# Kernel tuning notes

Hardware: AMD Instinct MI355X
Metric: run time of the kernel (lower is better)

Reference implementation:

```python
import jax, jax.numpy as jnp
import numpy as np

D_MODEL = 768
N_HEADS = 12
HEAD_DIM = D_MODEL // N_HEADS
FFN_DIM = 3072
MAX_WAVELENGTH = 10000.0
ROPE_PERCENT = 0.5
NORM_EPS = 1e-5


def setup_inputs() -> dict:
    key = jax.random.key(0)
    ks = jax.random.split(key, 12)
    B, C, S = 2, 16, 128
    init = lambda k, shape: (jax.random.normal(k, shape, dtype=jnp.float32) * 0.02)
    return {
        "hidden_state": jax.random.normal(ks[0], (B, C, S, D_MODEL), dtype=jnp.float32),
        "wq": init(ks[1], (D_MODEL, D_MODEL)), "bq": jnp.zeros((D_MODEL,), jnp.float32),
        "wk": init(ks[2], (D_MODEL, D_MODEL)), "bk": jnp.zeros((D_MODEL,), jnp.float32),
        "wv": init(ks[3], (D_MODEL, D_MODEL)), "bv": jnp.zeros((D_MODEL,), jnp.float32),
        "wo": init(ks[4], (D_MODEL, D_MODEL)), "bo": jnp.zeros((D_MODEL,), jnp.float32),
        "attn_biases": init(ks[5], (N_HEADS, 2)),
        "ln1_g": jnp.ones((D_MODEL,), jnp.float32), "ln1_b": jnp.zeros((D_MODEL,), jnp.float32),
        "ln3_g": jnp.ones((D_MODEL,), jnp.float32), "ln3_b": jnp.zeros((D_MODEL,), jnp.float32),
        "w1": init(ks[6], (D_MODEL, FFN_DIM)), "b1": jnp.zeros((FFN_DIM,), jnp.float32),
        "w2": init(ks[7], (FFN_DIM, D_MODEL)), "b2": jnp.zeros((D_MODEL,), jnp.float32),
    }


def _layernorm(x, g, b):
    mu = jnp.mean(x, axis=-1, keepdims=True)
    var = jnp.mean(jnp.square(x - mu), axis=-1, keepdims=True)
    return (x - mu) * jax.lax.rsqrt(var + NORM_EPS) * g + b


def _apply_p_rope(x, positions):
    # x: [B, H, T, head_dim]; p-RoPE: only rope_percent of frequency bands rotate.
    half = HEAD_DIM // 2
    rope_angles = int(ROPE_PERCENT * HEAD_DIM) // 2  # 16
    fraction = 2.0 * jnp.arange(rope_angles, dtype=jnp.float32) / HEAD_DIM
    timescale = jnp.concatenate([
        MAX_WAVELENGTH ** fraction,
        jnp.full((half - rope_angles,), jnp.inf, dtype=jnp.float32),
    ])  # [half]
    angles = positions[:, None].astype(jnp.float32) / timescale[None, :]  # [T, half]
    sin = jnp.sin(angles)[None, None]  # [1,1,T,half]
    cos = jnp.cos(angles)[None, None]
    x1, x2 = jnp.split(x, 2, axis=-1)
    return jnp.concatenate([x1 * cos - x2 * sin, x2 * cos + x1 * sin], axis=-1)


def _forward(hidden_state, wq, bq, wk, bk, wv, bv, wo, bo, attn_biases,
             ln1_g, ln1_b, ln3_g, ln3_b, w1, b1, w2, b2):
    B, C, S, D = hidden_state.shape
    T = C * S
    flat = hidden_state.reshape(B, T, D)

    # --- attention sublayer (pre-norm) ---
    ni = _layernorm(flat, ln1_g, ln1_b)
    scaling = HEAD_DIM ** -0.5
    q = (ni @ wq + bq) * scaling
    k = ni @ wk + bk
    v = ni @ wv + bv
    to_heads = lambda t: t.reshape(B, T, N_HEADS, HEAD_DIM).transpose(0, 2, 1, 3)
    q, k, v = to_heads(q), to_heads(k), to_heads(v)  # [B,H,T,hd]

    positions = jnp.arange(T)
    k = _apply_p_rope(k, positions)
    q = _apply_p_rope(q, positions)

    scores = jnp.einsum("bhtd,bhsd->bhts", q, k)  # [B,H,T,T]
    variate_ids = positions // S
    same = (variate_ids[:, None] == variate_ids[None, :]).astype(scores.dtype)  # [T,T]
    variate_bias = (same[None, :, :] * attn_biases[:, 0][:, None, None]
                    + (1.0 - same[None, :, :]) * attn_biases[:, 1][:, None, None])  # [H,T,T]
    scores = scores + variate_bias[None]
    probs = jax.nn.softmax(scores, axis=-1)
    attn = jnp.einsum("bhts,bhsd->bhtd", probs, v)
    attn = attn.transpose(0, 2, 1, 3).reshape(B, T, D)
    attn = attn @ wo + bo

    flat = flat + attn  # residual (pre-norm -> no post-norm here)

    # --- feed-forward sublayer (pre-norm) ---
    ff_in = _layernorm(flat, ln3_g, ln3_b)
    ff = jax.nn.gelu(ff_in @ w1 + b1, approximate=False) @ w2 + b2
    flat = flat + ff

    return flat.reshape(B, C, S, D)


def reference(hidden_state, wq, bq, wk, bk, wv, bv, wo, bo, attn_biases,
              ln1_g, ln1_b, ln3_g, ln3_b, w1, b1, w2, b2):
    return _forward(hidden_state, wq, bq, wk, bk, wv, bv, wo, bo, attn_biases,
                    ln1_g, ln1_b, ln3_g, ln3_b, w1, b1, w2, b2)
```

## Files before the change

kernel.cpp:

```cpp
#include <hip/hip_runtime.h>
#include <cmath>


typedef __bf16 bf16_t;
typedef bf16_t bf16x8 __attribute__((ext_vector_type(8)));
typedef float floatx4 __attribute__((ext_vector_type(4)));

#define MFMA(a, b, c) __builtin_amdgcn_mfma_f32_16x16x32_bf16((a), (b), (c), 0, 0, 0)
#define LOG2E 1.44269504088896340736f

__device__ __forceinline__ bf16_t f2bf(float f) { return (bf16_t)f; }

__device__ __forceinline__ void g2l16(const void* g, void* l) {
  __builtin_amdgcn_global_load_lds(
      (const __attribute__((address_space(1))) unsigned int*)g,
      (__attribute__((address_space(3))) unsigned int*)l, 16, 0, 0);
}

__device__ __forceinline__ void lds_fence() {
  asm volatile("s_waitcnt lgkmcnt(0)" ::: "memory");
}

struct PrepP {
  const float *wq, *wk, *wv, *wo, *w1, *w2;
  bf16_t *wqkvT, *woT, *w1T, *w2T;
  const float *hs, *g1, *be1;
  bf16_t* ni;
};

__global__ __launch_bounds__(256) void k_prep(PrepP p) {
  __shared__ float shm[32 * 33];
  const int bid = blockIdx.x;
  if (bid < 6912) {
    const float* in;
    bf16_t* out;
    int R, C, tx, ty;
    if (bid < 2304) {
      int m = bid / 576, lo = bid % 576;
      in = (m == 0) ? p.wq : (m == 1) ? p.wk : (m == 2) ? p.wv : p.wo;
      out = (m < 3) ? p.wqkvT + (size_t)m * 768 * 768 : p.woT;
      R = 768; C = 768; tx = lo % 24; ty = lo / 24;
    } else if (bid < 4608) {
      int lo = bid - 2304;
      in = p.w1; out = p.w1T; R = 768; C = 3072; tx = lo % 96; ty = lo / 96;
    } else {
      int lo = bid - 4608;
      in = p.w2; out = p.w2T; R = 3072; C = 768; tx = lo % 24; ty = lo / 24;
    }
    const int c0 = tx * 32, r0 = ty * 32;
    const int lx = threadIdx.x & 31, ly = threadIdx.x >> 5;
#pragma unroll
    for (int p4 = 0; p4 < 4; p4++) {
      int r = ly + p4 * 8;
      shm[r * 33 + lx] = in[(size_t)(r0 + r) * C + c0 + lx];
    }
    __syncthreads();
#pragma unroll
    for (int p4 = 0; p4 < 4; p4++) {
      int r = ly + p4 * 8;
      out[(size_t)(c0 + r) * R + r0 + lx] = f2bf(shm[lx * 33 + r]);
    }
  } else {
    const int row = bid - 6912;
    const float* xr = p.hs + (size_t)row * 768;
    const int t = threadIdx.x;
    float v0 = xr[t], v1 = xr[t + 256], v2 = xr[t + 512];
    float s = v0 + v1 + v2;
    float s2 = v0 * v0 + v1 * v1 + v2 * v2;
#pragma unroll
    for (int off = 32; off; off >>= 1) {
      s += __shfl_xor(s, off);
      s2 += __shfl_xor(s2, off);
    }
    const int w = t >> 6;
    if ((t & 63) == 0) { shm[w] = s; shm[4 + w] = s2; }
    __syncthreads();
    s = shm[0] + shm[1] + shm[2] + shm[3];
    s2 = shm[4] + shm[5] + shm[6] + shm[7];
    const float mu = s * (1.0f / 768.0f);
    const float var = s2 * (1.0f / 768.0f) - mu * mu;
    const float rstd = rsqrtf(var + 1e-5f);
    bf16_t* orow = p.ni + (size_t)row * 768;
    orow[t]       = f2bf((v0 - mu) * rstd * p.g1[t]       + p.be1[t]);
    orow[t + 256] = f2bf((v1 - mu) * rstd * p.g1[t + 256] + p.be1[t + 256]);
    orow[t + 512] = f2bf((v2 - mu) * rstd * p.g1[t + 512] + p.be1[t + 512]);
  }
}

__global__ __launch_bounds__(256) void k_layernorm(
    const float* __restrict__ x, const float* __restrict__ g,
    const float* __restrict__ b, bf16_t* __restrict__ out) {
  const int row = blockIdx.x;
  const float* xr = x + (size_t)row * 768;
  const int t = threadIdx.x;
  float v0 = xr[t], v1 = xr[t + 256], v2 = xr[t + 512];
  float s = v0 + v1 + v2;
  float s2 = v0 * v0 + v1 * v1 + v2 * v2;
#pragma unroll
  for (int off = 32; off; off >>= 1) {
    s += __shfl_xor(s, off);
    s2 += __shfl_xor(s2, off);
  }
  __shared__ float ra[4], rb[4];
  const int w = t >> 6;
  if ((t & 63) == 0) { ra[w] = s; rb[w] = s2; }
  __syncthreads();
  s = ra[0] + ra[1] + ra[2] + ra[3];
  s2 = rb[0] + rb[1] + rb[2] + rb[3];
  const float mu = s * (1.0f / 768.0f);
  const float var = s2 * (1.0f / 768.0f) - mu * mu;
  const float rstd = rsqrtf(var + 1e-5f);
  bf16_t* orow = out + (size_t)row * 768;
  orow[t]       = f2bf((v0 - mu) * rstd * g[t]       + b[t]);
  orow[t + 256] = f2bf((v1 - mu) * rstd * g[t + 256] + b[t + 256]);
  orow[t + 512] = f2bf((v2 - mu) * rstd * g[t + 512] + b[t + 512]);
}

struct GemmP {
  const bf16_t* A;
  const bf16_t* Bt;
  int M, N, K, mode;
  const float* bias0;
  const float* bias1;
  const float* bias2;
  float* outF;
  bf16_t* outB0;
  bf16_t* outB1;
  bf16_t* outB2;
};

__global__ __launch_bounds__(256, 2) void k_gemm(GemmP p) {
  __shared__ bf16_t lds[32768];
  const int tid = threadIdx.x;
  const int lane = tid & 63, wave = tid >> 6;
  const int quad = lane >> 4, l15 = lane & 15;
  const int wm = (wave >> 1) * 64, wn = (wave & 1) * 64;
  const int m0 = blockIdx.y * 128, n0 = blockIdx.x * 128;

  const char* gA[4];
  const char* gB[4];
#pragma unroll
  for (int pp = 0; pp < 4; pp++) {
    int slot = wave * 256 + pp * 64 + lane;
    int r = slot >> 3;
    int c8 = ((slot & 7) ^ (r & 7)) << 3;
    gA[pp] = (const char*)(p.A + (size_t)(m0 + r) * p.K + c8);
    gB[pp] = (const char*)(p.Bt + (size_t)(n0 + r) * p.K + c8);
  }

  int offA[4], offB[4];
#pragma unroll
  for (int i = 0; i < 4; i++) {
    int ra = wm + i * 16 + l15;
    offA[i] = ra * 64 + ((quad * 8) ^ ((ra & 7) << 3));
    int rb = wn + i * 16 + l15;
    offB[i] = rb * 64 + ((quad * 8) ^ ((rb & 7) << 3));
  }

  const floatx4 z4 = {0.f, 0.f, 0.f, 0.f};
  floatx4 acc[4][4];
#pragma unroll
  for (int i = 0; i < 4; i++)
#pragma unroll
    for (int j = 0; j < 4; j++) acc[i][j] = z4;

  const int KT = p.K >> 6;
  {
    bf16_t* A0 = lds + wave * 2048;
    bf16_t* B0 = lds + 16384 + wave * 2048;
#pragma unroll
    for (int pp = 0; pp < 4; pp++) {
      g2l16(gA[pp], A0 + pp * 512);
      g2l16(gB[pp], B0 + pp * 512);
    }
  }
  __syncthreads();

  for (int kt = 0; kt < KT; kt++) {
    const int cur = kt & 1;
    if (kt + 1 < KT) {
      const size_t kb = (size_t)(kt + 1) * 128;
      bf16_t* A1 = lds + (cur ^ 1) * 8192 + wave * 2048;
      bf16_t* B1 = lds + 16384 + (cur ^ 1) * 8192 + wave * 2048;
#pragma unroll
      for (int pp = 0; pp < 4; pp++) {
        g2l16(gA[pp] + kb, A1 + pp * 512);
        g2l16(gB[pp] + kb, B1 + pp * 512);
      }
    }
    const bf16_t* A0 = lds + cur * 8192;
    const bf16_t* B0 = lds + 16384 + cur * 8192;
#pragma unroll
    for (int ks = 0; ks < 2; ks++) {
      bf16x8 af[4], bfr[4];
#pragma unroll
      for (int i = 0; i < 4; i++) {
        af[i] = *(const bf16x8*)(A0 + (offA[i] ^ (ks * 32)));
        bfr[i] = *(const bf16x8*)(B0 + (offB[i] ^ (ks * 32)));
      }
#pragma unroll
      for (int i = 0; i < 4; i++)
#pragma unroll
        for (int j = 0; j < 4; j++) acc[i][j] = MFMA(af[i], bfr[j], acc[i][j]);
    }
    __syncthreads();
  }

  char* scr = (char*)lds + wave * 16384;

  if (p.mode == 0) {
    const int gnw = n0 + wn;
    const int region = gnw / 768;
    const int rem = gnw - region * 768;
    const int h = rem >> 6;
    const int b = (m0 + wm) >> 11;
    const int t0 = (m0 + wm) & 2047;
    const float* bias = (region == 0) ? p.bias0 : (region == 1 ? p.bias1 : p.bias2);
    float bb[4];
#pragma unroll
    for (int j = 0; j < 4; j++) bb[j] = bias[h * 64 + j * 16 + l15];
    bf16_t* sb = (bf16_t*)scr;
    if (region < 2) {
      const float scale = (region == 0) ? 0.125f * LOG2E : 1.0f;
      const float inv_ts = exp2f(-(float)l15 * (13.287712379549449f / 32.0f));
#pragma unroll
      for (int i = 0; i < 4; i++) {
#pragma unroll
        for (int reg = 0; reg < 4; reg++) {
          int tl = i * 16 + quad * 4 + reg;
          float sn, cs;
          __sincosf((float)(t0 + tl) * inv_ts, &sn, &cs);
          float v0 = (acc[i][0][reg] + bb[0]) * scale;
          float v1 = (acc[i][1][reg] + bb[1]) * scale;
          float v2 = (acc[i][2][reg] + bb[2]) * scale;
          float v3 = (acc[i][3][reg] + bb[3]) * scale;
          sb[tl * 72 + l15]      = f2bf(v0 * cs - v2 * sn);
          sb[tl * 72 + 16 + l15] = f2bf(v1);
          sb[tl * 72 + 32 + l15] = f2bf(v2 * cs + v0 * sn);
          sb[tl * 72 + 48 + l15] = f2bf(v3);
        }
      }
      __syncthreads();
      bf16_t* outp = (region == 0) ? p.outB0 : p.outB1;
      bf16_t* ob = outp + (((size_t)(b * 12 + h) * 2048 + t0) << 6);
#pragma unroll
      for (int pp = 0; pp < 8; pp++) {
        int row = pp * 8 + (lane >> 3), ch = (lane & 7) << 3;
        *(bf16x8*)(ob + row * 64 + ch) = *(const bf16x8*)&sb[row * 72 + ch];
      }
    } else {
#pragma unroll
      for (int i = 0; i < 4; i++)
#pragma unroll
        for (int j = 0; j < 4; j++)
#pragma unroll
          for (int reg = 0; reg < 4; reg++)
            sb[(j * 16 + l15) * 72 + i * 16 + quad * 4 + reg] =
                f2bf(acc[i][j][reg] + bb[j]);
      __syncthreads();
      bf16_t* ob = p.outB2 + (((size_t)(b * 12 + h)) << 17) + t0;
#pragma unroll
      for (int pp = 0; pp < 8; pp++) {
        int d = pp * 8 + (lane >> 3), ch = (lane & 7) << 3;
        *(bf16x8*)(ob + (size_t)d * 2048 + ch) = *(const bf16x8*)&sb[d * 72 + ch];
      }
    }
  } else {
    bf16_t* sb = (bf16_t*)scr;
    float bb[4];
#pragma unroll
    for (int j = 0; j < 4; j++) bb[j] = p.bias0[n0 + wn + j * 16 + l15];
#pragma unroll
    for (int i = 0; i < 4; i++)
#pragma unroll
      for (int j = 0; j < 4; j++)
#pragma unroll
        for (int reg = 0; reg < 4; reg++) {
          int tl = i * 16 + quad * 4 + reg;
          float x = acc[i][j][reg] + bb[j];
          float gv = 0.5f * x * (1.0f + erff(x * 0.70710678118654752f));
          sb[tl * 72 + j * 16 + l15] = f2bf(gv);
        }
    __syncthreads();
#pragma unroll
    for (int pp = 0; pp < 8; pp++) {
      int row = pp * 8 + (lane >> 3), ch = (lane & 7) << 3;
      *(bf16x8*)(p.outB0 + (size_t)(m0 + wm + row) * p.N + n0 + wn + ch) =
          *(const bf16x8*)&sb[row * 72 + ch];
    }
  }
}

__global__ __launch_bounds__(256, 3) void k_gemm64(
    const bf16_t* __restrict__ A, const bf16_t* __restrict__ Bt, int N, int K,
    const float* __restrict__ bias, const float* __restrict__ resid,
    float* __restrict__ outF) {
  __shared__ bf16_t lds[16384];
  const int tid = threadIdx.x;
  const int lane = tid & 63, wave = tid >> 6;
  const int quad = lane >> 4, l15 = lane & 15;
  const int wm = (wave >> 1) * 32, wn = (wave & 1) * 32;
  const int m0 = blockIdx.y * 64, n0 = blockIdx.x * 64;

  const char* gA[2];
  const char* gB[2];
#pragma unroll
  for (int pp = 0; pp < 2; pp++) {
    int slot = wave * 128 + pp * 64 + lane;
    int r = slot >> 3;
    int c8 = ((slot & 7) ^ (r & 7)) << 3;
    gA[pp] = (const char*)(A + (size_t)(m0 + r) * K + c8);
    gB[pp] = (const char*)(Bt + (size_t)(n0 + r) * K + c8);
  }

  int offA[2], offB[2];
#pragma unroll
  for (int i = 0; i < 2; i++) {
    int ra = wm + i * 16 + l15;
    offA[i] = ra * 64 + ((quad * 8) ^ ((ra & 7) << 3));
    int rb = wn + i * 16 + l15;
    offB[i] = rb * 64 + ((quad * 8) ^ ((rb & 7) << 3));
  }

  const floatx4 z4 = {0.f, 0.f, 0.f, 0.f};
  floatx4 acc[2][2];
#pragma unroll
  for (int i = 0; i < 2; i++)
#pragma unroll
    for (int j = 0; j < 2; j++) acc[i][j] = z4;

  const int KT = K >> 6;
  {
    bf16_t* A0 = lds + wave * 1024;
    bf16_t* B0 = lds + 8192 + wave * 1024;
#pragma unroll
    for (int pp = 0; pp < 2; pp++) {
      g2l16(gA[pp], A0 + pp * 512);
      g2l16(gB[pp], B0 + pp * 512);
    }
  }
  __syncthreads();

  for (int kt = 0; kt < KT; kt++) {
    const int cur = kt & 1;
    if (kt + 1 < KT) {
      const size_t kb = (size_t)(kt + 1) * 128;
      bf16_t* A1 = lds + (cur ^ 1) * 4096 + wave * 1024;
      bf16_t* B1 = lds + 8192 + (cur ^ 1) * 4096 + wave * 1024;
#pragma unroll
      for (int pp = 0; pp < 2; pp++) {
        g2l16(gA[pp] + kb, A1 + pp * 512);
        g2l16(gB[pp] + kb, B1 + pp * 512);
      }
    }
    const bf16_t* A0 = lds + cur * 4096;
    const bf16_t* B0 = lds + 8192 + cur * 4096;
#pragma unroll
    for (int ks = 0; ks < 2; ks++) {
      bf16x8 af[2], bfr[2];
#pragma unroll
      for (int i = 0; i < 2; i++) {
        af[i] = *(const bf16x8*)(A0 + (offA[i] ^ (ks * 32)));
        bfr[i] = *(const bf16x8*)(B0 + (offB[i] ^ (ks * 32)));
      }
#pragma unroll
      for (int i = 0; i < 2; i++)
#pragma unroll
        for (int j = 0; j < 2; j++) acc[i][j] = MFMA(af[i], bfr[j], acc[i][j]);
    }
    __syncthreads();
  }

  float* s4 = (float*)lds + wave * 1024;
#pragma unroll
  for (int i = 0; i < 2; i++)
#pragma unroll
    for (int j = 0; j < 2; j++)
#pragma unroll
      for (int reg = 0; reg < 4; reg++)
        s4[(i * 16 + quad * 4 + reg) * 32 + j * 16 + l15] = acc[i][j][reg];
  __syncthreads();
#pragma unroll
  for (int pp = 0; pp < 4; pp++) {
    int row = pp * 8 + (lane >> 3);
    int c4 = (lane & 7) * 4;
    floatx4 v = *(const floatx4*)&s4[row * 32 + c4];
    size_t goff = (size_t)(m0 + wm + row) * N + n0 + wn + c4;
    floatx4 rv = *(const floatx4*)(resid + goff);
    floatx4 bv = *(const floatx4*)(bias + n0 + wn + c4);
    *(floatx4*)(outF + goff) = v + rv + bv;
  }
}

__global__ __launch_bounds__(256, 3) void k_flash(
    const bf16_t* __restrict__ qh, const bf16_t* __restrict__ kh,
    const bf16_t* __restrict__ vt, const float* __restrict__ ab,
    bf16_t* __restrict__ attnA) {
  __shared__ bf16_t sm[20480];
  bf16_t* lK = sm;
  bf16_t* lV = sm + 8192;
  bf16_t* lP = sm + 16384;

  const int tid = threadIdx.x, lane = tid & 63, wave = tid >> 6;
  const int quad = lane >> 4, l15 = lane & 15;
  const int qtile = blockIdx.x, bh = blockIdx.y;
  const int h = bh % 12, bq = bh / 12;
  const int qr0 = qtile * 64 + wave * 16;

  const bf16_t* Qb = qh + (size_t)bh * 2048 * 64;
  const bf16_t* Kb = kh + (size_t)bh * 2048 * 64;
  const bf16_t* Vb = vt + (size_t)bh * 64 * 2048;

  const char* gK[2];
  const char* gV[2];
#pragma unroll
  for (int pp = 0; pp < 2; pp++) {
    int slot = wave * 128 + pp * 64 + lane;
    int r = slot >> 3;
    int c8 = ((slot & 7) ^ (r & 7)) << 3;
    gK[pp] = (const char*)(Kb + r * 64 + c8);
    gV[pp] = (const char*)(Vb + (size_t)r * 2048 + c8);
  }

  bf16x8 qf[2];
#pragma unroll
  for (int ks = 0; ks < 2; ks++)
    qf[ks] = *(const bf16x8*)(Qb + (size_t)(qr0 + l15) * 64 + ks * 32 + quad * 8);

  int offK[4];
#pragma unroll
  for (int t4 = 0; t4 < 4; t4++) {
    int sr = t4 * 16 + l15;
    offK[t4] = sr * 64 + ((quad * 8) ^ ((sr & 7) << 3));
  }
  const int offP = l15 * 64 + ((quad * 8) ^ ((l15 & 7) << 3));

  const floatx4 z4 = {0.f, 0.f, 0.f, 0.f};
  float l_all[4] = {0.f, 0.f, 0.f, 0.f};
  float l_same[4] = {0.f, 0.f, 0.f, 0.f};
  floatx4 oacc[4], osame[4];
#pragma unroll
  for (int dt = 0; dt < 4; dt++) { oacc[dt] = z4; osame[dt] = z4; }

  const float f_s = exp2f(ab[h * 2] * LOG2E);
  const float f_d = exp2f(ab[h * 2 + 1] * LOG2E);
  const int myv = qtile >> 1;

  {
    bf16_t* K0 = lK + wave * 1024;
    bf16_t* V0 = lV + wave * 1024;
#pragma unroll
    for (int pp = 0; pp < 2; pp++) {
      g2l16(gK[pp], K0 + pp * 512);
      g2l16(gV[pp], V0 + pp * 512);
    }
  }
  __syncthreads();

  for (int kv = 0; kv < 32; kv++) {
    const int cur = kv & 1;
    if (kv + 1 < 32) {
      bf16_t* K1 = lK + (cur ^ 1) * 4096 + wave * 1024;
      bf16_t* V1 = lV + (cur ^ 1) * 4096 + wave * 1024;
      const size_t kb = (size_t)(kv + 1) * 8192, vb = (size_t)(kv + 1) * 128;
#pragma unroll
      for (int pp = 0; pp < 2; pp++) {
        g2l16(gK[pp] + kb, K1 + pp * 512);
        g2l16(gV[pp] + vb, V1 + pp * 512);
      }
    }
    const bf16_t* K0 = lK + cur * 4096;
    const bf16_t* V0 = lV + cur * 4096;

    floatx4 sacc[4] = {z4, z4, z4, z4};
#pragma unroll
    for (int ks = 0; ks < 2; ks++)
#pragma unroll
      for (int ct = 0; ct < 4; ct++)
        sacc[ct] = MFMA(qf[ks], *(const bf16x8*)(K0 + (offK[ct] ^ (ks * 32))),
                        sacc[ct]);

    const bool same = ((kv >> 1) == myv);

#pragma unroll
    for (int ct = 0; ct < 4; ct++)
#pragma unroll
      for (int reg = 0; reg < 4; reg++) {
        float pv = exp2f(sacc[ct][reg]);
        sacc[ct][reg] = pv;
        l_all[reg] += pv;
      }
    if (same) {
#pragma unroll
      for (int ct = 0; ct < 4; ct++)
#pragma unroll
        for (int reg = 0; reg < 4; reg++) l_same[reg] += sacc[ct][reg];
    }

    bf16_t* myP = lP + wave * 1024;
#pragma unroll
    for (int ct = 0; ct < 4; ct++)
#pragma unroll
      for (int reg = 0; reg < 4; reg++) {
        int r = quad * 4 + reg, s = ct * 16 + l15;
        myP[r * 64 + (((s >> 3) ^ (r & 7)) << 3) + (s & 7)] =
            f2bf(sacc[ct][reg]);
      }
    lds_fence();

    bf16x8 pf[2];
#pragma unroll
    for (int ks = 0; ks < 2; ks++)
      pf[ks] = *(const bf16x8*)(myP + (offP ^ (ks * 32)));
#pragma unroll
    for (int ks = 0; ks < 2; ks++)
#pragma unroll
      for (int dt = 0; dt < 4; dt++)
        oacc[dt] = MFMA(pf[ks], *(const bf16x8*)(V0 + (offK[dt] ^ (ks * 32))),
                        oacc[dt]);
    if (same) {
#pragma unroll
      for (int ks = 0; ks < 2; ks++)
#pragma unroll
        for (int dt = 0; dt < 4; dt++)
          osame[dt] = MFMA(pf[ks], *(const bf16x8*)(V0 + (offK[dt] ^ (ks * 32))),
                           osame[dt]);
    }
    __syncthreads();
  }

  const float df = f_s - f_d;
  float inv_l[4];
#pragma unroll
  for (int reg = 0; reg < 4; reg++) {
    float la = l_all[reg], ls = l_same[reg];
    la += __shfl_xor(la, 1); la += __shfl_xor(la, 2);
    la += __shfl_xor(la, 4); la += __shfl_xor(la, 8);
    ls += __shfl_xor(ls, 1); ls += __shfl_xor(ls, 2);
    ls += __shfl_xor(ls, 4); ls += __shfl_xor(ls, 8);
    inv_l[reg] = 1.0f / (f_d * la + df * ls);
  }

  bf16_t* myP = lP + wave * 1024;
#pragma unroll
  for (int dt = 0; dt < 4; dt++)
#pragma unroll
    for (int reg = 0; reg < 4; reg++)
      myP[(quad * 4 + reg) * 64 + dt * 16 + l15] =
          f2bf((f_d * oacc[dt][reg] + df * osame[dt][reg]) * inv_l[reg]);
  __syncthreads();
#pragma unroll
  for (int pp = 0; pp < 2; pp++) {
    int row = pp * 8 + (lane >> 3), ch = (lane & 7) << 3;
    *(bf16x8*)(attnA + ((size_t)(bq * 2048 + qr0 + row)) * 768 + h * 64 + ch) =
        *(const bf16x8*)&myP[row * 64 + ch];
  }
}

extern "C" void kernel_launch(void* const* d_in, const int* in_sizes, int n_in,
                              void* d_out, int out_size, void* d_ws,
                              size_t ws_size, hipStream_t stream) {
  const float* hs  = (const float*)d_in[0];
  const float* wq  = (const float*)d_in[1];
  const float* bq  = (const float*)d_in[2];
  const float* wk  = (const float*)d_in[3];
  const float* bk  = (const float*)d_in[4];
  const float* wv  = (const float*)d_in[5];
  const float* bv  = (const float*)d_in[6];
  const float* wo  = (const float*)d_in[7];
  const float* bo  = (const float*)d_in[8];
  const float* ab  = (const float*)d_in[9];
  const float* g1  = (const float*)d_in[10];
  const float* be1 = (const float*)d_in[11];
  const float* g3  = (const float*)d_in[12];
  const float* be3 = (const float*)d_in[13];
  const float* w1  = (const float*)d_in[14];
  const float* b1  = (const float*)d_in[15];
  const float* w2  = (const float*)d_in[16];
  const float* b2  = (const float*)d_in[17];

  char* ws = (char*)d_ws;
  size_t off = 0;
  auto alloc = [&](size_t bytes) -> void* {
    void* p = ws + off;
    off += (bytes + 255) & ~(size_t)255;
    return p;
  };
  bf16_t* wqkvT = (bf16_t*)alloc((size_t)2304 * 768 * 2);
  bf16_t* woT   = (bf16_t*)alloc((size_t)768 * 768 * 2);
  bf16_t* w1T   = (bf16_t*)alloc((size_t)3072 * 768 * 2);
  bf16_t* w2T   = (bf16_t*)alloc((size_t)768 * 3072 * 2);
  bf16_t* ni    = (bf16_t*)alloc((size_t)4096 * 768 * 2);
  bf16_t* qhB   = (bf16_t*)alloc((size_t)24 * 2048 * 64 * 2);
  bf16_t* khB   = (bf16_t*)alloc((size_t)24 * 2048 * 64 * 2);
  bf16_t* vtB   = (bf16_t*)alloc((size_t)24 * 64 * 2048 * 2);
  bf16_t* attnA = (bf16_t*)alloc((size_t)4096 * 768 * 2);
  float*  resid1 = (float*)alloc((size_t)4096 * 768 * 4);
  bf16_t* ffn1o = qhB;

  PrepP pp = {wq, wk, wv, wo, w1, w2, wqkvT, woT, w1T, w2T, hs, g1, be1, ni};
  k_prep<<<11008, 256, 0, stream>>>(pp);

  GemmP gqkv = {ni, wqkvT, 4096, 2304, 768, 0,
                bq, bk, bv, nullptr, qhB, khB, vtB};
  k_gemm<<<dim3(18, 32), 256, 0, stream>>>(gqkv);

  k_flash<<<dim3(32, 24), 256, 0, stream>>>(qhB, khB, vtB, ab, attnA);

  k_gemm64<<<dim3(12, 64), 256, 0, stream>>>(attnA, woT, 768, 768, bo, hs,
                                             resid1);

  k_layernorm<<<4096, 256, 0, stream>>>(resid1, g3, be3, ni);

  GemmP gf1 = {ni, w1T, 4096, 3072, 768, 2,
               b1, nullptr, nullptr, nullptr, ffn1o, nullptr, nullptr};
  k_gemm<<<dim3(24, 32), 256, 0, stream>>>(gf1);

  k_gemm64<<<dim3(12, 64), 256, 0, stream>>>(ffn1o, w2T, 768, 3072, b2,
                                             resid1, (float*)d_out);
}
```

Before: 294.9 us.

## Single-buffer GEMM LDS for occupancy and fold variate bias into attention exponent

Both GEMM kernels drop double-buffered LDS prefetch in favour of a single buffer with load-then-sync, shrinking shared memory and raising launch-bounds occupancy. The 64-tile GEMM also doubles its K-step to 128 with a new swizzle. The attention kernel adds the per-head variate bias directly inside exp2, replacing the separate same-variate accumulator, l_same sums and extra MFMAs. The trade-off is that global-to-LDS loads no longer overlap compute within a block, so latency hiding now depends on more resident blocks.

```diff
diff --git a/kernel.cpp b/kernel.cpp
--- a/kernel.cpp
+++ b/kernel.cpp
@@ -129,8 +129,8 @@
   bf16_t* outB2;
 };
 
-__global__ __launch_bounds__(256, 2) void k_gemm(GemmP p) {
-  __shared__ bf16_t lds[32768];
+__global__ __launch_bounds__(256, 3) void k_gemm(GemmP p) {
+  __shared__ bf16_t lds[18432];
   const int tid = threadIdx.x;
   const int lane = tid & 63, wave = tid >> 6;
   const int quad = lane >> 4, l15 = lane & 15;
@@ -165,38 +165,24 @@
     for (int j = 0; j < 4; j++) acc[i][j] = z4;
 
   const int KT = p.K >> 6;
-  {
-    bf16_t* A0 = lds + wave * 2048;
-    bf16_t* B0 = lds + 16384 + wave * 2048;
+  bf16_t* Ad = lds + wave * 2048;
+  bf16_t* Bd = lds + 8192 + wave * 2048;
+
+  for (int kt = 0; kt < KT; kt++) {
+    const size_t kb = (size_t)kt * 128;
 #pragma unroll
     for (int pp = 0; pp < 4; pp++) {
-      g2l16(gA[pp], A0 + pp * 512);
-      g2l16(gB[pp], B0 + pp * 512);
-    }
-  }
-  __syncthreads();
-
-  for (int kt = 0; kt < KT; kt++) {
-    const int cur = kt & 1;
-    if (kt + 1 < KT) {
-      const size_t kb = (size_t)(kt + 1) * 128;
-      bf16_t* A1 = lds + (cur ^ 1) * 8192 + wave * 2048;
-      bf16_t* B1 = lds + 16384 + (cur ^ 1) * 8192 + wave * 2048;
-#pragma unroll
-      for (int pp = 0; pp < 4; pp++) {
-        g2l16(gA[pp] + kb, A1 + pp * 512);
-        g2l16(gB[pp] + kb, B1 + pp * 512);
-      }
-    }
-    const bf16_t* A0 = lds + cur * 8192;
-    const bf16_t* B0 = lds + 16384 + cur * 8192;
+      g2l16(gA[pp] + kb, Ad + pp * 512);
+      g2l16(gB[pp] + kb, Bd + pp * 512);
+    }
+    __syncthreads();
 #pragma unroll
     for (int ks = 0; ks < 2; ks++) {
       bf16x8 af[4], bfr[4];
 #pragma unroll
       for (int i = 0; i < 4; i++) {
-        af[i] = *(const bf16x8*)(A0 + (offA[i] ^ (ks * 32)));
-        bfr[i] = *(const bf16x8*)(B0 + (offB[i] ^ (ks * 32)));
+        af[i] = *(const bf16x8*)(lds + (offA[i] ^ (ks * 32)));
+        bfr[i] = *(const bf16x8*)(lds + 8192 + (offB[i] ^ (ks * 32)));
       }
 #pragma unroll
       for (int i = 0; i < 4; i++)
@@ -206,7 +192,7 @@
     __syncthreads();
   }
 
-  char* scr = (char*)lds + wave * 16384;
+  char* scr = (char*)lds + wave * 9216;
 
   if (p.mode == 0) {
     const int gnw = n0 + wn;
@@ -291,7 +277,7 @@
   }
 }
 
-__global__ __launch_bounds__(256, 3) void k_gemm64(
+__global__ __launch_bounds__(256, 4) void k_gemm64(
     const bf16_t* __restrict__ A, const bf16_t* __restrict__ Bt, int N, int K,
     const float* __restrict__ bias, const float* __restrict__ resid,
     float* __restrict__ outF) {
@@ -302,24 +288,15 @@
   const int wm = (wave >> 1) * 32, wn = (wave & 1) * 32;
   const int m0 = blockIdx.y * 64, n0 = blockIdx.x * 64;
 
-  const char* gA[2];
-  const char* gB[2];
-#pragma unroll
-  for (int pp = 0; pp < 2; pp++) {
-    int slot = wave * 128 + pp * 64 + lane;
-    int r = slot >> 3;
-    int c8 = ((slot & 7) ^ (r & 7)) << 3;
-    gA[pp] = (const char*)(A + (size_t)(m0 + r) * K + c8);
-    gB[pp] = (const char*)(Bt + (size_t)(n0 + r) * K + c8);
-  }
-
-  int offA[2], offB[2];
-#pragma unroll
-  for (int i = 0; i < 2; i++) {
-    int ra = wm + i * 16 + l15;
-    offA[i] = ra * 64 + ((quad * 8) ^ ((ra & 7) << 3));
-    int rb = wn + i * 16 + l15;
-    offB[i] = rb * 64 + ((quad * 8) ^ ((rb & 7) << 3));
+  const char* gA[4];
+  const char* gB[4];
+#pragma unroll
+  for (int pp = 0; pp < 4; pp++) {
+    int slot = wave * 256 + pp * 64 + lane;
+    int r = slot >> 4;
+    int c = ((slot & 15) ^ (r & 7)) << 3;
+    gA[pp] = (const char*)(A + (size_t)(m0 + r) * K + c);
+    gB[pp] = (const char*)(Bt + (size_t)(n0 + r) * K + c);
   }
 
   const floatx4 z4 = {0.f, 0.f, 0.f, 0.f};
@@ -329,39 +306,29 @@
 #pragma unroll
     for (int j = 0; j < 2; j++) acc[i][j] = z4;
 
-  const int KT = K >> 6;
-  {
-    bf16_t* A0 = lds + wave * 1024;
-    bf16_t* B0 = lds + 8192 + wave * 1024;
-#pragma unroll
-    for (int pp = 0; pp < 2; pp++) {
-      g2l16(gA[pp], A0 + pp * 512);
-      g2l16(gB[pp], B0 + pp * 512);
-    }
-  }
-  __syncthreads();
+  const int KT = K >> 7;
+  bf16_t* Ad = lds + wave * 2048;
+  bf16_t* Bd = lds + 8192 + wave * 2048;
 
   for (int kt = 0; kt < KT; kt++) {
-    const int cur = kt & 1;
-    if (kt + 1 < KT) {
-      const size_t kb = (size_t)(kt + 1) * 128;
-      bf16_t* A1 = lds + (cur ^ 1) * 4096 + wave * 1024;
-      bf16_t* B1 = lds + 8192 + (cur ^ 1) * 4096 + wave * 1024;
-#pragma unroll
-      for (int pp = 0; pp < 2; pp++) {
-        g2l16(gA[pp] + kb, A1 + pp * 512);
-        g2l16(gB[pp] + kb, B1 + pp * 512);
-      }
-    }
-    const bf16_t* A0 = lds + cur * 4096;
-    const bf16_t* B0 = lds + 8192 + cur * 4096;
-#pragma unroll
-    for (int ks = 0; ks < 2; ks++) {
+    const size_t kb = (size_t)kt * 256;
+#pragma unroll
+    for (int pp = 0; pp < 4; pp++) {
+      g2l16(gA[pp] + kb, Ad + pp * 512);
+      g2l16(gB[pp] + kb, Bd + pp * 512);
+    }
+    __syncthreads();
+#pragma unroll
+    for (int ks = 0; ks < 4; ks++) {
       bf16x8 af[2], bfr[2];
 #pragma unroll
       for (int i = 0; i < 2; i++) {
-        af[i] = *(const bf16x8*)(A0 + (offA[i] ^ (ks * 32)));
-        bfr[i] = *(const bf16x8*)(B0 + (offB[i] ^ (ks * 32)));
+        int ra = wm + i * 16 + l15;
+        af[i] = *(const bf16x8*)(lds + ra * 128 +
+                                 (((ks * 4 + quad) ^ (ra & 7)) << 3));
+        int rb = wn + i * 16 + l15;
+        bfr[i] = *(const bf16x8*)(lds + 8192 + rb * 128 +
+                                  (((ks * 4 + quad) ^ (rb & 7)) << 3));
       }
 #pragma unroll
       for (int i = 0; i < 2; i++)
@@ -437,13 +404,12 @@
 
   const floatx4 z4 = {0.f, 0.f, 0.f, 0.f};
   float l_all[4] = {0.f, 0.f, 0.f, 0.f};
-  float l_same[4] = {0.f, 0.f, 0.f, 0.f};
-  floatx4 oacc[4], osame[4];
-#pragma unroll
-  for (int dt = 0; dt < 4; dt++) { oacc[dt] = z4; osame[dt] = z4; }
-
-  const float f_s = exp2f(ab[h * 2] * LOG2E);
-  const float f_d = exp2f(ab[h * 2 + 1] * LOG2E);
+  floatx4 oacc[4];
+#pragma unroll
+  for (int dt = 0; dt < 4; dt++) oacc[dt] = z4;
+
+  const float bc_same = ab[h * 2] * LOG2E;
+  const float bc_diff = ab[h * 2 + 1] * LOG2E;
   const int myv = qtile >> 1;
 
   {
@@ -480,22 +446,15 @@
         sacc[ct] = MFMA(qf[ks], *(const bf16x8*)(K0 + (offK[ct] ^ (ks * 32))),
                         sacc[ct]);
 
-    const bool same = ((kv >> 1) == myv);
-
+    const float bc = ((kv >> 1) == myv) ? bc_same : bc_diff;
 #pragma unroll
     for (int ct = 0; ct < 4; ct++)
 #pragma unroll
       for (int reg = 0; reg < 4; reg++) {
-        float pv = exp2f(sacc[ct][reg]);
+        float pv = exp2f(sacc[ct][reg] + bc);
         sacc[ct][reg] = pv;
         l_all[reg] += pv;
       }
-    if (same) {
-#pragma unroll
-      for (int ct = 0; ct < 4; ct++)
-#pragma unroll
-        for (int reg = 0; reg < 4; reg++) l_same[reg] += sacc[ct][reg];
-    }
 
     bf16_t* myP = lP + wave * 1024;
 #pragma unroll
@@ -508,37 +467,24 @@
       }
     lds_fence();
 
-    bf16x8 pf[2];
-#pragma unroll
-    for (int ks = 0; ks < 2; ks++)
-      pf[ks] = *(const bf16x8*)(myP + (offP ^ (ks * 32)));
-#pragma unroll
-    for (int ks = 0; ks < 2; ks++)
+#pragma unroll
+    for (int ks = 0; ks < 2; ks++) {
+      bf16x8 pf = *(const bf16x8*)(myP + (offP ^ (ks * 32)));
 #pragma unroll
       for (int dt = 0; dt < 4; dt++)
-        oacc[dt] = MFMA(pf[ks], *(const bf16x8*)(V0 + (offK[dt] ^ (ks * 32))),
+        oacc[dt] = MFMA(pf, *(const bf16x8*)(V0 + (offK[dt] ^ (ks * 32))),
                         oacc[dt]);
-    if (same) {
-#pragma unroll
-      for (int ks = 0; ks < 2; ks++)
-#pragma unroll
-        for (int dt = 0; dt < 4; dt++)
-          osame[dt] = MFMA(pf[ks], *(const bf16x8*)(V0 + (offK[dt] ^ (ks * 32))),
-                           osame[dt]);
-    }
-    __syncthreads();
-  }
-
-  const float df = f_s - f_d;
+    }
+    __syncthreads();
+  }
+
   float inv_l[4];
 #pragma unroll
   for (int reg = 0; reg < 4; reg++) {
-    float la = l_all[reg], ls = l_same[reg];
+    float la = l_all[reg];
     la += __shfl_xor(la, 1); la += __shfl_xor(la, 2);
     la += __shfl_xor(la, 4); la += __shfl_xor(la, 8);
-    ls += __shfl_xor(ls, 1); ls += __shfl_xor(ls, 2);
-    ls += __shfl_xor(ls, 4); ls += __shfl_xor(ls, 8);
-    inv_l[reg] = 1.0f / (f_d * la + df * ls);
+    inv_l[reg] = 1.0f / la;
   }
 
   bf16_t* myP = lP + wave * 1024;
@@ -547,7 +493,7 @@
 #pragma unroll
     for (int reg = 0; reg < 4; reg++)
       myP[(quad * 4 + reg) * 64 + dt * 16 + l15] =
-          f2bf((f_d * oacc[dt][reg] + df * osame[dt][reg]) * inv_l[reg]);
+          f2bf(oacc[dt][reg] * inv_l[reg]);
   __syncthreads();
 #pragma unroll
   for (int pp = 0; pp < 2; pp++) {
```

After: 290.8 us. About the same (-1.4%).
